# Kernel tuning notes

Hardware: AMD Instinct MI355X
Metric: run time of the kernel (lower is better)

The kernel has to match this reference:

```python
import jax, jax.numpy as jnp
import numpy as np

B, CHAN, HW = 256, 3, 32
NC, DIM = 10, 48
FC1_IN = (HW - 4) * (HW - 4) * 64 // 4  # 12544


def _signed_root(m, a, p, b):
    # sign(sign(m)+0.1) * ((|m|+a)^p - b)
    return jnp.sign(jnp.sign(m) + 0.1) * (jnp.power(jnp.abs(m) + a, p) - b)


def setup_inputs() -> dict:
    key = jax.random.key(0)
    ks = jax.random.split(key, 12)
    f32 = jnp.float32
    x = jax.random.normal(ks[0], (B, CHAN, HW, HW), f32)
    conv1_w = jax.random.normal(ks[1], (32, CHAN, 3, 3), f32) * (1.0 / np.sqrt(CHAN * 9))
    conv1_b = jax.random.normal(ks[2], (32,), f32) * 0.01
    conv2_w = jax.random.normal(ks[3], (64, 32, 3, 3), f32) * (1.0 / np.sqrt(32 * 9))
    conv2_b = jax.random.normal(ks[4], (64,), f32) * 0.01
    fc1_w = jax.random.normal(ks[5], (128, FC1_IN), f32) * (1.0 / np.sqrt(FC1_IN))
    fc1_b = jax.random.normal(ks[6], (128,), f32) * 0.01
    fc2_w = jax.random.normal(ks[7], (128, 128), f32) * (1.0 / np.sqrt(128))
    fc2_b = jax.random.normal(ks[8], (128,), f32) * 0.01
    fc3_w = jax.random.normal(ks[9], (DIM, 128), f32) * (1.0 / np.sqrt(128))
    fc3_b = jax.random.normal(ks[10], (DIM,), f32) * 0.01
    centers = jnp.eye(NC, DIM, dtype=f32)
    # GaussMoments constants: standard-normal joint moments (non-trainable)
    mom_weight = jnp.ones((DIM,), f32)          # order-1 moment weights, reused for all orders in source
    gm1 = jnp.zeros((DIM,), f32)                # E[z_i] = 0
    eye = jnp.eye(DIM, dtype=f32)
    gm2 = eye                                   # E[z_i z_j] = delta_ij
    gm3 = jnp.zeros((DIM, DIM, DIM), f32)       # odd moments vanish
    gm4 = (eye[:, :, None, None] * eye[None, None, :, :]
           + eye[:, None, :, None] * eye[None, :, None, :]
           + eye[:, None, None, :] * eye[None, :, :, None])  # Isserlis
    return {"x": x, "conv1_w": conv1_w, "conv1_b": conv1_b, "conv2_w": conv2_w,
            "conv2_b": conv2_b, "fc1_w": fc1_w, "fc1_b": fc1_b, "fc2_w": fc2_w,
            "fc2_b": fc2_b, "fc3_w": fc3_w, "fc3_b": fc3_b, "centers": centers,
            "mom_weight": mom_weight, "gm1": gm1, "gm2": gm2, "gm3": gm3, "gm4": gm4}


def _backbone(x, c1w, c1b, c2w, c2b, f1w, f1b, f2w, f2b, f3w, f3b):
    dn = ("NCHW", "OIHW", "NCHW")
    h = jax.lax.conv_general_dilated(x, c1w, (1, 1), "VALID", dimension_numbers=dn)
    h = jax.nn.relu(h + c1b[None, :, None, None])
    h = jax.lax.conv_general_dilated(h, c2w, (1, 1), "VALID", dimension_numbers=dn)
    h = jax.nn.relu(h + c2b[None, :, None, None])
    h = jax.lax.reduce_window(h, -jnp.inf, jax.lax.max, (1, 1, 2, 2), (1, 1, 2, 2), "VALID")
    h = h.reshape(h.shape[0], -1)
    h = jax.nn.relu(h @ f1w.T + f1b)
    h = jax.nn.relu(h @ f2w.T + f2b)
    return h @ f3w.T + f3b  # [B, DIM]


def _gmm_tail(z, centers, mom_weight, gm1, gm2, gm3, gm4):
    Bv, d, C = z.shape[0], DIM, NC
    diff = z[:, None, :] - centers[None, :, :]              # [B,C,d]
    dist_sq = jnp.sum(diff * diff, axis=-1)                 # [B,C]
    expo = -0.5 * dist_sq
    expo_safe = expo - jnp.max(expo, axis=1, keepdims=True)  # MaxPool1d(10) == max over classes
    numer_safe = jnp.exp(expo_safe)
    resp = numer_safe / jnp.sum(numer_safe, axis=1, keepdims=True)
    onehot = jax.nn.one_hot(jnp.argmin(dist_sq, axis=-1), C, dtype=diff.dtype)  # [B,C]
    do = diff * onehot[:, :, None]                          # [B,C,d]
    cw = jnp.sum(onehot, axis=0)                            # [C]
    eps = 1e-7
    m1 = jnp.sum(do, axis=0) / (cw[:, None] + eps)          # [C,d]
    pair = jnp.einsum("bci,bcj->bcij", do, do).reshape(Bv, C, d * d)  # [B,C,d^2]
    m2 = jnp.sum(pair, axis=0).reshape(C, d, d) / (cw[:, None, None] + eps)
    m3 = jnp.einsum("bcp,bck->cpk", pair, do).reshape(C, d, d, d)      # NOT count-normalized (as in source)
    m4 = jnp.einsum("bcp,bcq->cpq", pair, pair).reshape(C, d, d, d, d)  # NOT count-normalized (as in source)
    m2 = _signed_root(m2, 0.25, 0.5, 0.5)
    m3 = _signed_root(m3, 0.19245008973, 0.3333333333, 0.57735026919)
    m4 = _signed_root(m4, 0.15749013123, 0.25, 0.62996052494)
    t1 = gm1
    t2 = _signed_root(gm2, 0.25, 0.5, 0.5)
    t3 = _signed_root(gm3, 0.19245008973, 0.3333333333, 0.57735026919)
    t4 = _signed_root(gm4, 0.15749013123, 0.25, 0.62996052494)
    cwn = cw / jnp.sum(cw)
    # moment weights broadcast over the LAST axis only (torch repeat semantics in source)
    p1 = jnp.sum(cwn[:, None] * mom_weight * (m1 - t1[None]) ** 2)
    p2 = jnp.sum(cwn[:, None, None] * mom_weight * (m2 - t2[None]) ** 2)
    p3 = jnp.sum(cwn[:, None, None, None] * mom_weight * (m3 - t3[None]) ** 2)
    p4 = jnp.sum(cwn[:, None, None, None, None] * mom_weight * (m4 - t4[None]) ** 2)
    log_resp = jnp.log(jnp.clip(resp, 1e-8))
    return log_resp, p1, p2, p3, p4


def reference(x, conv1_w, conv1_b, conv2_w, conv2_b, fc1_w, fc1_b, fc2_w, fc2_b,
              fc3_w, fc3_b, centers, mom_weight, gm1, gm2, gm3, gm4):
    z = _backbone(x, conv1_w, conv1_b, conv2_w, conv2_b, fc1_w, fc1_b, fc2_w, fc2_b, fc3_w, fc3_b)
    return _gmm_tail(z, centers, mom_weight, gm1, gm2, gm3, gm4)
```

## Files before the change

### kernel.cpp

```cpp
#include <hip/hip_runtime.h>
#include <math.h>

#define BATCH   256
#define NCLS    10
#define DIM     48

#define OFF_H1B   0
#define OFF_PAIR  0
#define OFF_FC1P  602112
#define OFF_WT    2699264
#define OFF_PTFH  4500000
#define OFF_PTFL  5300000
#define OFF_POOL  7372800
#define OFF_DO    10596352
#define OFF_CW    10608640
#define OFF_INT   10608656
#define OFF_WPH   10612000
#define OFF_WPL   10622000

typedef __attribute__((ext_vector_type(8))) short short8;
typedef __attribute__((ext_vector_type(4))) float floatx4;
typedef unsigned short u16;
typedef unsigned int u32;

__device__ __forceinline__ u16 f2bf(float v) {
    u32 u = __float_as_uint(v);
    return (u16)((u + 0x7fffu + ((u >> 16) & 1u)) >> 16);
}
__device__ __forceinline__ float bf2f(u16 h) {
    return __uint_as_float(((u32)h) << 16);
}

__device__ __forceinline__ float sroot_half(float m) {
    float s = (m < 0.f) ? -1.f : 1.f;
    return s * (sqrtf(fabsf(m) + 0.25f) - 0.5f);
}
__device__ __forceinline__ float sroot_cbrt(float m) {
    float s = (m < 0.f) ? -1.f : 1.f;
    return s * (cbrtf(fabsf(m) + 0.19245008973f) - 0.57735026919f);
}
__device__ __forceinline__ float sroot_quarter(float m) {
    float s = (m < 0.f) ? -1.f : 1.f;
    return s * (sqrtf(sqrtf(fabsf(m) + 0.15749013123f)) - 0.62996052494f);
}

__global__ void k_conv1(const float* __restrict__ x, const float* __restrict__ w,
                        const float* __restrict__ bias, u16* __restrict__ h1b,
                        const float* __restrict__ c2w, u16* __restrict__ wph,
                        u16* __restrict__ wpl, float* __restrict__ cw,
                        int* __restrict__ cls_cnt, float* __restrict__ out) {
    int blk = blockIdx.x;
    int tid = threadIdx.x;
    if (blk == 900) {
        for (int i = tid; i < 18432; i += 256) {
            int icr = i & 7, rest = i >> 3;
            int oc = rest & 63, rest2 = rest >> 6;
            int icq = rest2 & 3, s = rest2 >> 2;
            int ic = icq * 8 + icr;
            float v = c2w[(oc * 32 + ic) * 9 + s];
            u16 hi = f2bf(v);
            wph[i] = hi;
            wpl[i] = f2bf(v - bf2f(hi));
        }
        return;
    }
    if (blk == 0) {
        if (tid < 16) { cw[tid] = 0.f; cls_cnt[tid] = 0; }
        else if (tid < 20) out[2560 + tid - 16] = 0.f;
    }
    int pos = blk * 256 + tid;
    int b = pos / 900, rem = pos % 900;
    int y = rem / 30, xx = rem % 30;
    float win[27];
#pragma unroll
    for (int ic = 0; ic < 3; ic++)
#pragma unroll
        for (int ky = 0; ky < 3; ky++)
#pragma unroll
            for (int kx = 0; kx < 3; kx++)
                win[ic * 9 + ky * 3 + kx] = x[b * 3072 + ic * 1024 + (y + ky) * 32 + xx + kx];
    u16* hp = h1b + (size_t)pos * 64;
#pragma unroll
    for (int ch = 0; ch < 4; ch++) {
        u32 hiw[4], low[4];
#pragma unroll
        for (int a2 = 0; a2 < 4; a2++) {
            u16 h2[2], l2[2];
#pragma unroll
            for (int e = 0; e < 2; e++) {
                int oc = ch * 8 + a2 * 2 + e;
                float s = bias[oc];
#pragma unroll
                for (int k = 0; k < 27; k++) s = fmaf(win[k], w[oc * 27 + k], s);
                s = fmaxf(s, 0.f);
                u16 hi = f2bf(s);
                h2[e] = hi;
                l2[e] = f2bf(s - bf2f(hi));
            }
            hiw[a2] = (u32)h2[0] | ((u32)h2[1] << 16);
            low[a2] = (u32)l2[0] | ((u32)l2[1] << 16);
        }
        *(uint4*)(hp + ch * 8)      = make_uint4(hiw[0], hiw[1], hiw[2], hiw[3]);
        *(uint4*)(hp + 32 + ch * 8) = make_uint4(low[0], low[1], low[2], low[3]);
    }
}

__global__ void k_conv2(const u16* __restrict__ h1b, const u16* __restrict__ wph,
                        const u16* __restrict__ wpl, const float* __restrict__ bias,
                        float* __restrict__ pooled) {
    __shared__ u16 hs[256 * 72];
    int blk = blockIdx.x;
    int b = blk >> 2, sub = blk & 3;
    int hy = sub >> 1, hx = sub & 1;
    int row0 = hy * 14, col0 = hx * 14;
    int tid = threadIdx.x;
    for (int i = tid; i < 2048; i += 256) {
        int p = i >> 3, c8 = i & 7;
        int r = p >> 4, cc = p & 15;
        size_t gp = (size_t)b * 900 + (size_t)(row0 + r) * 30 + col0 + cc;
        *(uint4*)(&hs[p * 72 + c8 * 8]) = *(const uint4*)(&h1b[gp * 64 + c8 * 8]);
    }
    int wv = tid >> 6, lane = tid & 63;
    int n = lane & 15, quad = lane >> 4;
    int ocb = wv * 16 + n;
    float bv = bias[ocb];
    short8 bh[9], bl[9];
#pragma unroll
    for (int s = 0; s < 9; s++) {
        int off = (((s * 4 + quad) * 64) + ocb) * 8;
        bh[s] = *(const short8*)(&wph[off]);
        bl[s] = *(const short8*)(&wpl[off]);
    }
    __syncthreads();
    int ml = lane & 15;
    for (int t = 0; t < 13; t++) {
        int gA = t * 4 + (ml >> 2);
        int d = ml & 3;
        int gc = (gA < 49) ? gA : 0;
        int py = gc / 7, px = gc % 7;
        int rb = 2 * py + (d >> 1), cb = 2 * px + (d & 1);
        floatx4 acc = {0.f, 0.f, 0.f, 0.f};
#pragma unroll
        for (int s = 0; s < 9; s++) {
            int ky = s / 3, kx = s % 3;
            int pos = (rb + ky) * 16 + cb + kx;
            short8 ah = *(const short8*)(&hs[pos * 72 + quad * 8]);
            short8 al = *(const short8*)(&hs[pos * 72 + 32 + quad * 8]);
            acc = __builtin_amdgcn_mfma_f32_16x16x32_bf16(ah, bh[s], acc, 0, 0, 0);
            acc = __builtin_amdgcn_mfma_f32_16x16x32_bf16(ah, bl[s], acc, 0, 0, 0);
            acc = __builtin_amdgcn_mfma_f32_16x16x32_bf16(al, bh[s], acc, 0, 0, 0);
        }
        int G = t * 4 + quad;
        if (G < 49) {
            float v = fmaxf(fmaxf(acc.x, acc.y), fmaxf(acc.z, acc.w));
            v = fmaxf(v + bv, 0.f);
            int pyg = hy * 7 + G / 7, pxg = hx * 7 + G % 7;
            pooled[(size_t)b * 12544 + ocb * 196 + pyg * 14 + pxg] = v;
        }
    }
}

__global__ void k_wtrans(const float* __restrict__ w, float* __restrict__ wT) {
    __shared__ float tile[32][33];
    int kb = blockIdx.x % 392, nb = blockIdx.x / 392;
    int tid = threadIdx.x;
    int tx = tid & 31, ty = tid >> 5;
    int k0 = kb * 32, n0 = nb * 32;
#pragma unroll
    for (int r = 0; r < 4; r++)
        tile[tx][ty * 4 + r] = w[(n0 + ty * 4 + r) * 12544 + k0 + tx];
    __syncthreads();
#pragma unroll
    for (int r = 0; r < 4; r++)
        wT[(k0 + ty * 4 + r) * 128 + n0 + tx] = tile[ty * 4 + r][tx];
}

__global__ void k_fc1(const float* __restrict__ pooled, const float* __restrict__ wT,
                      float* __restrict__ fc1p) {
    __shared__ __align__(16) float Alds[16 * 196];
    int blk = blockIdx.x;
    int sg = blk >> 6, kc = blk & 63;
    int tid = threadIdx.x;
    int m0 = sg * 16, k0 = kc * 196;
    for (int i = tid; i < 784; i += 256) {
        int m = i / 49, u = i % 49;
        ((float4*)Alds)[m * 49 + u] = ((const float4*)(pooled + (m0 + m) * 12544 + k0))[u];
    }
    __syncthreads();
    int n2 = tid & 63, mg = tid >> 6;
    const float* wp = wT + (size_t)k0 * 128 + n2;
    const float* arow = Alds + mg * 4 * 196;
    float acc[4][2];
#pragma unroll
    for (int j = 0; j < 4; j++) { acc[j][0] = 0.f; acc[j][1] = 0.f; }
    for (int k = 0; k < 196; k += 2) {
        float wa0 = wp[k * 128],        wb0 = wp[k * 128 + 64];
        float wa1 = wp[(k + 1) * 128],  wb1 = wp[(k + 1) * 128 + 64];
#pragma unroll
        for (int j = 0; j < 4; j++) {
            float2 av = *(const float2*)(arow + j * 196 + k);
            acc[j][0] = fmaf(av.x, wa0, acc[j][0]);
            acc[j][0] = fmaf(av.y, wa1, acc[j][0]);
            acc[j][1] = fmaf(av.x, wb0, acc[j][1]);
            acc[j][1] = fmaf(av.y, wb1, acc[j][1]);
        }
    }
#pragma unroll
    for (int j = 0; j < 4; j++) {
        int m = m0 + mg * 4 + j;
        fc1p[kc * 32768 + m * 128 + n2]      = acc[j][0];
        fc1p[kc * 32768 + m * 128 + n2 + 64] = acc[j][1];
    }
}

__global__ void k_fc23a(const float* __restrict__ fc1p, const float* __restrict__ f1b,
                        const float* __restrict__ w2, const float* __restrict__ b2,
                        const float* __restrict__ w3, const float* __restrict__ b3,
                        const float* __restrict__ centers, float* __restrict__ out,
                        float* __restrict__ dov, float* __restrict__ pairm,
                        float* __restrict__ cw, int* __restrict__ cls_cnt,
                        int* __restrict__ cls_idx) {
    __shared__ float a[128], h[128], zb[48], dvs[48];
    __shared__ float dist[10];
    __shared__ float smn, ssum;
    __shared__ int sarg;
    int b = blockIdx.x, t = threadIdx.x;
    float s0 = f1b[t];
    for (int p = 0; p < 64; p++) s0 += fc1p[p * 32768 + b * 128 + t];
    a[t] = fmaxf(s0, 0.f);
    __syncthreads();
    float s = b2[t];
    const float* wr = w2 + t * 128;
#pragma unroll 4
    for (int k = 0; k < 128; k++) s = fmaf(wr[k], a[k], s);
    h[t] = fmaxf(s, 0.f);
    __syncthreads();
    if (t < 48) {
        float s3 = b3[t];
        const float* wr3 = w3 + t * 128;
#pragma unroll 4
        for (int k = 0; k < 128; k++) s3 = fmaf(wr3[k], h[k], s3);
        zb[t] = s3;
    }
    __syncthreads();
    if (t < 10) {
        float d = 0.f;
        const float* cc = centers + t * 48;
        for (int k = 0; k < 48; k++) { float df = zb[k] - cc[k]; d = fmaf(df, df, d); }
        dist[t] = d;
    }
    __syncthreads();
    if (t == 0) {
        float mn = dist[0]; int arg = 0;
        for (int c = 1; c < 10; c++) if (dist[c] < mn) { mn = dist[c]; arg = c; }
        float sum = 0.f;
        for (int c = 0; c < 10; c++) sum += expf(-0.5f * (dist[c] - mn));
        smn = mn; ssum = sum; sarg = arg;
        atomicAdd(&cw[arg], 1.f);
        int pos = atomicAdd(&cls_cnt[arg], 1);
        cls_idx[arg * 256 + pos] = b;
    }
    __syncthreads();
    if (t < 10) {
        float es = -0.5f * (dist[t] - smn);
        float resp = expf(es) / ssum;
        out[b * 10 + t] = logf(fmaxf(resp, 1e-8f));
    }
    if (t < 48) {
        float v = zb[t] - centers[sarg * 48 + t];
        dvs[t] = v;
        dov[b * 48 + t] = v;
    }
    __syncthreads();
#pragma unroll
    for (int e = 0; e < 18; e++) {
        int cell = t + 128 * e;
        pairm[b * 2304 + cell] = dvs[cell / 48] * dvs[cell % 48];
    }
}

__global__ void k_prep(const float* __restrict__ pairm, const float* __restrict__ dov,
                       const float* __restrict__ cw, const int* __restrict__ cls_cnt,
                       const int* __restrict__ cls_idx, const float* __restrict__ momw,
                       const float* __restrict__ gm1, const float* __restrict__ gm2,
                       const float* __restrict__ gm3, u16* __restrict__ ptfh,
                       u16* __restrict__ ptfl, float* __restrict__ out) {
    __shared__ __align__(16) float smem[7424];
    int blk = blockIdx.x;
    int t = threadIdx.x;

    if (blk < 648) {
        float* tile = smem;
        int* cmap = (int*)(smem + 2080);
        int ctile = blk / 18, coltile = blk % 18;
        int cell0 = ctile * 64, col0 = coltile * 32;
        if (t < 32) {
            int j = col0 + t, base = 0, samp = -1;
            for (int c = 0; c < 10; c++) {
                int cnt = cls_cnt[c];
                if (j >= base && j < base + cnt) samp = cls_idx[c * 256 + (j - base)];
                base += (cnt + 31) & ~31;
            }
            cmap[t] = samp;
        }
        __syncthreads();
        for (int i = t; i < 2048; i += 256) {
            int u = i >> 6, ce = i & 63;
            int s = cmap[u];
            tile[u * 65 + ce] = (s >= 0) ? pairm[(size_t)s * 2304 + cell0 + ce] : 0.f;
        }
        __syncthreads();
        int kc = col0 >> 5;
        int rt0 = cell0 >> 4;
        for (int o = t; o < 2048; o += 256) {
            int rtl = o >> 9, lane = (o >> 3) & 63, j = o & 7;
            int m = lane & 15, quad = lane >> 4;
            float v = tile[(quad * 8 + j) * 65 + rtl * 16 + m];
            u16 hi = f2bf(v);
            size_t off = ((size_t)((rt0 + rtl) * 18 + kc) * 64 + lane) * 8 + j;
            ptfh[off] = hi;
            ptfl[off] = f2bf(v - bf2f(hi));
        }

    } else if (blk < 1008) {
        float* Pl = smem;
        float* Dl = smem + 4096;
        float* red = smem + 7168;
        int bb = blk - 648;
        int c = bb / 36, pt = bb % 36;
        int cnt = cls_cnt[c];
        const int* cidx = cls_idx + c * 256;
        int pl = t >> 2, kq = t & 3;
        float acc[12];
#pragma unroll
        for (int m = 0; m < 12; m++) acc[m] = 0.f;
        for (int s0 = 0; s0 < cnt; s0 += 64) {
            int sc = min(64, cnt - s0);
            __syncthreads();
            for (int i = t; i < sc * 16; i += 256) {
                int row = i >> 4, u = i & 15;
                ((float4*)Pl)[row * 16 + u] =
                    ((const float4*)(pairm + (size_t)cidx[s0 + row] * 2304 + pt * 64))[u];
            }
            for (int i = t; i < sc * 12; i += 256) {
                int row = i / 12, u = i % 12;
                ((float4*)Dl)[row * 12 + u] =
                    ((const float4*)(dov + (size_t)cidx[s0 + row] * 48))[u];
            }
            __syncthreads();
            for (int s = 0; s < sc; s++) {
                float pa = Pl[s * 64 + pl];
                float4 d0 = *(const float4*)&Dl[s * 48 + kq * 12];
                float4 d1 = *(const float4*)&Dl[s * 48 + kq * 12 + 4];
                float4 d2 = *(const float4*)&Dl[s * 48 + kq * 12 + 8];
                acc[0]  = fmaf(pa, d0.x, acc[0]);  acc[1]  = fmaf(pa, d0.y, acc[1]);
                acc[2]  = fmaf(pa, d0.z, acc[2]);  acc[3]  = fmaf(pa, d0.w, acc[3]);
                acc[4]  = fmaf(pa, d1.x, acc[4]);  acc[5]  = fmaf(pa, d1.y, acc[5]);
                acc[6]  = fmaf(pa, d1.z, acc[6]);  acc[7]  = fmaf(pa, d1.w, acc[7]);
                acc[8]  = fmaf(pa, d2.x, acc[8]);  acc[9]  = fmaf(pa, d2.y, acc[9]);
                acc[10] = fmaf(pa, d2.z, acc[10]); acc[11] = fmaf(pa, d2.w, acc[11]);
            }
        }
        float cwn = cw[c] * (1.f / 256.f);
        int p = pt * 64 + pl;
        float p3c = 0.f;
#pragma unroll
        for (int m = 0; m < 12; m++) {
            int k = kq * 12 + m;
            float d3 = sroot_cbrt(acc[m]) - sroot_cbrt(gm3[p * 48 + k]);
            p3c += momw[k] * d3 * d3;
        }
        p3c *= cwn;
        red[t] = p3c; __syncthreads();
        for (int off = 128; off > 0; off >>= 1) { if (t < off) red[t] += red[t + off]; __syncthreads(); }
        if (t == 0) atomicAdd(&out[2562], red[0]);

    } else {
        float* ds = smem;
        float* red = smem + 3072;
        int bb = blk - 1008;
        int c = bb / 9, r = bb % 9;
        int cnt = cls_cnt[c];
        const int* cidx = cls_idx + c * 256;
        int cell = t + 256 * r;
        int ci = cell / 48, cj = cell % 48;
        float a0 = 0.f, a1 = 0.f, a2 = 0.f, a3 = 0.f;
        float m1a = 0.f, m1b = 0.f;
        for (int s0 = 0; s0 < cnt; s0 += 64) {
            int sc = min(64, cnt - s0);
            __syncthreads();
            for (int i = t; i < sc * 48; i += 256)
                ds[i] = dov[(size_t)cidx[s0 + i / 48] * 48 + (i % 48)];
            __syncthreads();
            int s = 0;
            for (; s + 4 <= sc; s += 4) {
                a0 = fmaf(ds[s * 48 + ci],       ds[s * 48 + cj],       a0);
                a1 = fmaf(ds[(s + 1) * 48 + ci], ds[(s + 1) * 48 + cj], a1);
                a2 = fmaf(ds[(s + 2) * 48 + ci], ds[(s + 2) * 48 + cj], a2);
                a3 = fmaf(ds[(s + 3) * 48 + ci], ds[(s + 3) * 48 + cj], a3);
            }
            for (; s < sc; s++) a0 = fmaf(ds[s * 48 + ci], ds[s * 48 + cj], a0);
            if (r == 0 && t < 48) {
                int ss = 0;
                for (; ss + 2 <= sc; ss += 2) {
                    m1a += ds[ss * 48 + t];
                    m1b += ds[(ss + 1) * 48 + t];
                }
                for (; ss < sc; ss++) m1a += ds[ss * 48 + t];
            }
        }
        float denom = cw[c] + 1e-7f;
        float cwn = cw[c] * (1.f / 256.f);
        float m2v = (a0 + a1 + a2 + a3) / denom;
        float d2 = sroot_half(m2v) - sroot_half(gm2[cell]);
        float p2c = cwn * momw[cj] * d2 * d2;
        __syncthreads();
        red[t] = p2c; __syncthreads();
        for (int off = 128; off > 0; off >>= 1) { if (t < off) red[t] += red[t + off]; __syncthreads(); }
        if (t == 0) atomicAdd(&out[2561], red[0]);
        if (r == 0 && t < 48) {
            float m1v = (m1a + m1b) / denom;
            float d1 = m1v - gm1[t];
            atomicAdd(&out[2560], cwn * momw[t] * d1 * d1);
        }
    }
}

__global__ __launch_bounds__(256, 4)
void k_p4(const u16* __restrict__ ptfh, const u16* __restrict__ ptfl,
          const float* __restrict__ cw, const int* __restrict__ cls_cnt,
          const float* __restrict__ momw, float* __restrict__ out) {
    __shared__ float red[256];
    int blk = blockIdx.x;
    int c = blk / 171;
    int cnt = cls_cnt[c];
    if (cnt == 0) return;
    int rem = blk % 171;
    int pt = 0;
    while (rem >= 18 - pt) { rem -= 18 - pt; pt++; }
    int qt = pt + rem;
    int kc0 = 0;
    for (int cc = 0; cc < c; cc++) kc0 += (cls_cnt[cc] + 31) >> 5;
    int kch = (cnt + 31) >> 5;
    int t = threadIdx.x;
    int w = t >> 6, lane = t & 63;
    int ml = lane & 15, quad = lane >> 4;
    floatx4 acc[16];
#pragma unroll
    for (int i = 0; i < 16; i++) acc[i] = (floatx4){0.f, 0.f, 0.f, 0.f};
    for (int kc = 0; kc < kch; kc++) {
        short8 ah[2], al[2];
#pragma unroll
        for (int ms = 0; ms < 2; ms++) {
            int art = pt * 8 + w * 2 + ms;
            size_t aoff = ((size_t)(art * 18 + kc0 + kc) * 64 + lane) * 8;
            ah[ms] = *(const short8*)(ptfh + aoff);
            al[ms] = *(const short8*)(ptfl + aoff);
        }
#pragma unroll
        for (int ns = 0; ns < 8; ns++) {
            int brt = qt * 8 + ns;
            size_t boff = ((size_t)(brt * 18 + kc0 + kc) * 64 + lane) * 8;
            short8 bhv = *(const short8*)(ptfh + boff);
            short8 blv = *(const short8*)(ptfl + boff);
#pragma unroll
            for (int ms = 0; ms < 2; ms++) {
                int id = ms * 8 + ns;
                acc[id] = __builtin_amdgcn_mfma_f32_16x16x32_bf16(ah[ms], bhv, acc[id], 0, 0, 0);
                acc[id] = __builtin_amdgcn_mfma_f32_16x16x32_bf16(ah[ms], blv, acc[id], 0, 0, 0);
                acc[id] = __builtin_amdgcn_mfma_f32_16x16x32_bf16(al[ms], bhv, acc[id], 0, 0, 0);
            }
        }
    }
    float T1 = sroot_quarter(1.f), T3 = sroot_quarter(3.f);
    float cwn = cw[c] * (1.f / 256.f);
    bool diag = (pt == qt);
    int ipv[8], jpv[8];
    float mwpv[8];
#pragma unroll
    for (int ms = 0; ms < 2; ms++)
#pragma unroll
        for (int reg = 0; reg < 4; reg++) {
            int p = (pt * 8 + w * 2 + ms) * 16 + quad * 4 + reg;
            ipv[ms * 4 + reg] = p / 48;
            jpv[ms * 4 + reg] = p % 48;
            mwpv[ms * 4 + reg] = momw[p % 48];
        }
    float p4c = 0.f;
#pragma unroll
    for (int ns = 0; ns < 8; ns++) {
        int q = (qt * 8 + ns) * 16 + ml;
        int kq = q / 48, lq = q % 48;
        float mq = momw[lq];
#pragma unroll
        for (int ms = 0; ms < 2; ms++) {
            int id = ms * 8 + ns;
#pragma unroll
            for (int reg = 0; reg < 4; reg++) {
                int ip = ipv[ms * 4 + reg], jp = jpv[ms * 4 + reg];
                int g = ((ip == jp) && (kq == lq))
                      + ((ip == kq) && (jp == lq))
                      + ((ip == lq) && (jp == kq));
                float t4v = (g == 0) ? 0.f : ((g == 1) ? T1 : T3);
                float d4 = sroot_quarter(acc[id][reg]) - t4v;
                float wgt = diag ? mq : (mq + mwpv[ms * 4 + reg]);
                p4c += wgt * d4 * d4;
            }
        }
    }
    p4c *= cwn;
    red[t] = p4c; __syncthreads();
    for (int off = 128; off > 0; off >>= 1) { if (t < off) red[t] += red[t + off]; __syncthreads(); }
    if (t == 0) atomicAdd(&out[2563], red[0]);
}

extern "C" void kernel_launch(void* const* d_in, const int* in_sizes, int n_in,
                              void* d_out, int out_size, void* d_ws, size_t ws_size,
                              hipStream_t stream) {
    const float* x    = (const float*)d_in[0];
    const float* c1w  = (const float*)d_in[1];
    const float* c1b  = (const float*)d_in[2];
    const float* c2w  = (const float*)d_in[3];
    const float* c2b  = (const float*)d_in[4];
    const float* f1w  = (const float*)d_in[5];
    const float* f1b  = (const float*)d_in[6];
    const float* f2w  = (const float*)d_in[7];
    const float* f2b  = (const float*)d_in[8];
    const float* f3w  = (const float*)d_in[9];
    const float* f3b  = (const float*)d_in[10];
    const float* cen  = (const float*)d_in[11];
    const float* momw = (const float*)d_in[12];
    const float* gm1  = (const float*)d_in[13];
    const float* gm2  = (const float*)d_in[14];
    const float* gm3  = (const float*)d_in[15];

    float* ws      = (float*)d_ws;
    u16*   h1b     = (u16*)(ws + OFF_H1B);
    float* pairm   = ws + OFF_PAIR;
    float* fc1p    = ws + OFF_FC1P;
    float* wT      = ws + OFF_WT;
    u16*   ptfh    = (u16*)(ws + OFF_PTFH);
    u16*   ptfl    = (u16*)(ws + OFF_PTFL);
    float* pooled  = ws + OFF_POOL;
    float* dov     = ws + OFF_DO;
    float* cwp     = ws + OFF_CW;
    int*   iws     = (int*)(ws + OFF_INT);
    int*   cls_cnt = iws;
    int*   cls_idx = iws + 16;
    u16*   wph     = (u16*)(ws + OFF_WPH);
    u16*   wpl     = (u16*)(ws + OFF_WPL);
    float* out     = (float*)d_out;

    k_conv1<<<901, 256, 0, stream>>>(x, c1w, c1b, h1b, c2w, wph, wpl,
                                     cwp, cls_cnt, out);
    k_conv2<<<1024, 256, 0, stream>>>(h1b, wph, wpl, c2b, pooled);
    k_wtrans<<<1568, 256, 0, stream>>>(f1w, wT);
    k_fc1<<<1024, 256, 0, stream>>>(pooled, wT, fc1p);
    k_fc23a<<<256, 128, 0, stream>>>(fc1p, f1b, f2w, f2b, f3w, f3b, cen, out,
                                     dov, pairm, cwp, cls_cnt, cls_idx);
    k_prep<<<1098, 256, 0, stream>>>(pairm, dov, cwp, cls_cnt, cls_idx, momw,
                                     gm1, gm2, gm3, ptfh, ptfl, out);
    k_p4<<<1710, 256, 0, stream>>>(ptfh, ptfl, cwp, cls_cnt, momw, out);
}
```

Before: 256.9 us.

## Fuse conv1 into conv2 kernel, computing conv1 tile in shared memory

Merges the conv1 and conv2 kernels. Each conv2 block now loads its 18x18x3 input patch into shared memory and computes the 16x16 conv1 halo tile (bf16 hi/lo split) straight into LDS, with no global h1 buffer. The conv2 weights are also split into bf16 hi/lo per thread inside the block instead of by a dedicated prep block. This removes one launch and the global write and read of the intermediate activation. In exchange, halo positions overlapping neighbouring sub-tiles are recomputed, and every block repeats the scattered weight conversion.

Result: slower. 265.9 us (+3.5%).

```diff
diff --git a/kernel.cpp b/kernel.cpp
--- a/kernel.cpp
+++ b/kernel.cpp
@@ -5,7 +5,6 @@
 #define NCLS    10
 #define DIM     48
 
-#define OFF_H1B   0
 #define OFF_PAIR  0
 #define OFF_FC1P  602112
 #define OFF_WT    2699264
@@ -15,8 +14,6 @@
 #define OFF_DO    10596352
 #define OFF_CW    10608640
 #define OFF_INT   10608656
-#define OFF_WPH   10612000
-#define OFF_WPL   10622000
 
 typedef __attribute__((ext_vector_type(8))) short short8;
 typedef __attribute__((ext_vector_type(4))) float floatx4;
@@ -44,92 +41,79 @@
     return s * (sqrtf(sqrtf(fabsf(m) + 0.15749013123f)) - 0.62996052494f);
 }
 
-__global__ void k_conv1(const float* __restrict__ x, const float* __restrict__ w,
-                        const float* __restrict__ bias, u16* __restrict__ h1b,
-                        const float* __restrict__ c2w, u16* __restrict__ wph,
-                        u16* __restrict__ wpl, float* __restrict__ cw,
-                        int* __restrict__ cls_cnt, float* __restrict__ out) {
+__global__ void k_conv12(const float* __restrict__ x, const float* __restrict__ c1w,
+                         const float* __restrict__ c1b, const float* __restrict__ c2w,
+                         const float* __restrict__ c2b, float* __restrict__ pooled,
+                         float* __restrict__ cw, int* __restrict__ cls_cnt,
+                         float* __restrict__ out) {
+    __shared__ u16 hs[256 * 72];
+    __shared__ float xs[972];
     int blk = blockIdx.x;
     int tid = threadIdx.x;
-    if (blk == 900) {
-        for (int i = tid; i < 18432; i += 256) {
-            int icr = i & 7, rest = i >> 3;
-            int oc = rest & 63, rest2 = rest >> 6;
-            int icq = rest2 & 3, s = rest2 >> 2;
-            int ic = icq * 8 + icr;
-            float v = c2w[(oc * 32 + ic) * 9 + s];
-            u16 hi = f2bf(v);
-            wph[i] = hi;
-            wpl[i] = f2bf(v - bf2f(hi));
-        }
-        return;
-    }
     if (blk == 0) {
         if (tid < 16) { cw[tid] = 0.f; cls_cnt[tid] = 0; }
         else if (tid < 20) out[2560 + tid - 16] = 0.f;
     }
-    int pos = blk * 256 + tid;
-    int b = pos / 900, rem = pos % 900;
-    int y = rem / 30, xx = rem % 30;
-    float win[27];
-#pragma unroll
-    for (int ic = 0; ic < 3; ic++)
-#pragma unroll
-        for (int ky = 0; ky < 3; ky++)
-#pragma unroll
-            for (int kx = 0; kx < 3; kx++)
-                win[ic * 9 + ky * 3 + kx] = x[b * 3072 + ic * 1024 + (y + ky) * 32 + xx + kx];
-    u16* hp = h1b + (size_t)pos * 64;
-#pragma unroll
-    for (int ch = 0; ch < 4; ch++) {
-        u32 hiw[4], low[4];
-#pragma unroll
-        for (int a2 = 0; a2 < 4; a2++) {
-            u16 h2[2], l2[2];
-#pragma unroll
-            for (int e = 0; e < 2; e++) {
-                int oc = ch * 8 + a2 * 2 + e;
-                float s = bias[oc];
-#pragma unroll
-                for (int k = 0; k < 27; k++) s = fmaf(win[k], w[oc * 27 + k], s);
-                s = fmaxf(s, 0.f);
-                u16 hi = f2bf(s);
-                h2[e] = hi;
-                l2[e] = f2bf(s - bf2f(hi));
-            }
-            hiw[a2] = (u32)h2[0] | ((u32)h2[1] << 16);
-            low[a2] = (u32)l2[0] | ((u32)l2[1] << 16);
-        }
-        *(uint4*)(hp + ch * 8)      = make_uint4(hiw[0], hiw[1], hiw[2], hiw[3]);
-        *(uint4*)(hp + 32 + ch * 8) = make_uint4(low[0], low[1], low[2], low[3]);
-    }
-}
-
-__global__ void k_conv2(const u16* __restrict__ h1b, const u16* __restrict__ wph,
-                        const u16* __restrict__ wpl, const float* __restrict__ bias,
-                        float* __restrict__ pooled) {
-    __shared__ u16 hs[256 * 72];
-    int blk = blockIdx.x;
     int b = blk >> 2, sub = blk & 3;
     int hy = sub >> 1, hx = sub & 1;
     int row0 = hy * 14, col0 = hx * 14;
-    int tid = threadIdx.x;
-    for (int i = tid; i < 2048; i += 256) {
-        int p = i >> 3, c8 = i & 7;
-        int r = p >> 4, cc = p & 15;
-        size_t gp = (size_t)b * 900 + (size_t)(row0 + r) * 30 + col0 + cc;
-        *(uint4*)(&hs[p * 72 + c8 * 8]) = *(const uint4*)(&h1b[gp * 64 + c8 * 8]);
+    for (int i = tid; i < 972; i += 256) {
+        int ic = i / 324, r2 = i % 324;
+        int rr = r2 / 18, cc = r2 % 18;
+        xs[i] = x[b * 3072 + ic * 1024 + (row0 + rr) * 32 + col0 + cc];
     }
     int wv = tid >> 6, lane = tid & 63;
     int n = lane & 15, quad = lane >> 4;
     int ocb = wv * 16 + n;
-    float bv = bias[ocb];
+    float bv = c2b[ocb];
     short8 bh[9], bl[9];
 #pragma unroll
     for (int s = 0; s < 9; s++) {
-        int off = (((s * 4 + quad) * 64) + ocb) * 8;
-        bh[s] = *(const short8*)(&wph[off]);
-        bl[s] = *(const short8*)(&wpl[off]);
+        short8 hv, lv;
+#pragma unroll
+        for (int j = 0; j < 8; j++) {
+            float v = c2w[(ocb * 32 + quad * 8 + j) * 9 + s];
+            u16 hi = f2bf(v);
+            hv[j] = (short)hi;
+            lv[j] = (short)f2bf(v - bf2f(hi));
+        }
+        bh[s] = hv; bl[s] = lv;
+    }
+    __syncthreads();
+    {
+        int r = tid >> 4, c = tid & 15;
+        float win[27];
+#pragma unroll
+        for (int ic = 0; ic < 3; ic++)
+#pragma unroll
+            for (int ky = 0; ky < 3; ky++)
+#pragma unroll
+                for (int kx = 0; kx < 3; kx++)
+                    win[ic * 9 + ky * 3 + kx] = xs[ic * 324 + (r + ky) * 18 + c + kx];
+        u16* hp = hs + tid * 72;
+#pragma unroll
+        for (int ch = 0; ch < 4; ch++) {
+            u32 hiw[4], low[4];
+#pragma unroll
+            for (int a2 = 0; a2 < 4; a2++) {
+                u16 h2[2], l2[2];
+#pragma unroll
+                for (int e = 0; e < 2; e++) {
+                    int oc = ch * 8 + a2 * 2 + e;
+                    float s = c1b[oc];
+#pragma unroll
+                    for (int k = 0; k < 27; k++) s = fmaf(win[k], c1w[oc * 27 + k], s);
+                    s = fmaxf(s, 0.f);
+                    u16 hi = f2bf(s);
+                    h2[e] = hi;
+                    l2[e] = f2bf(s - bf2f(hi));
+                }
+                hiw[a2] = (u32)h2[0] | ((u32)h2[1] << 16);
+                low[a2] = (u32)l2[0] | ((u32)l2[1] << 16);
+            }
+            *(uint4*)(hp + ch * 8)      = make_uint4(hiw[0], hiw[1], hiw[2], hiw[3]);
+            *(uint4*)(hp + 32 + ch * 8) = make_uint4(low[0], low[1], low[2], low[3]);
+        }
     }
     __syncthreads();
     int ml = lane & 15;
@@ -535,7 +519,6 @@
     const float* gm3  = (const float*)d_in[15];
 
     float* ws      = (float*)d_ws;
-    u16*   h1b     = (u16*)(ws + OFF_H1B);
     float* pairm   = ws + OFF_PAIR;
     float* fc1p    = ws + OFF_FC1P;
     float* wT      = ws + OFF_WT;
@@ -547,13 +530,10 @@
     int*   iws     = (int*)(ws + OFF_INT);
     int*   cls_cnt = iws;
     int*   cls_idx = iws + 16;
-    u16*   wph     = (u16*)(ws + OFF_WPH);
-    u16*   wpl     = (u16*)(ws + OFF_WPL);
     float* out     = (float*)d_out;
 
-    k_conv1<<<901, 256, 0, stream>>>(x, c1w, c1b, h1b, c2w, wph, wpl,
-                                     cwp, cls_cnt, out);
-    k_conv2<<<1024, 256, 0, stream>>>(h1b, wph, wpl, c2b, pooled);
+    k_conv12<<<1024, 256, 0, stream>>>(x, c1w, c1b, c2w, c2b, pooled,
+                                       cwp, cls_cnt, out);
     k_wtrans<<<1568, 256, 0, stream>>>(f1w, wT);
     k_fc1<<<1024, 256, 0, stream>>>(pooled, wT, fc1p);
     k_fc23a<<<256, 128, 0, stream>>>(fc1p, f1b, f2w, f2b, f3w, f3b, cen, out,
```
